# Performance work log

Measured on AMD Instinct MI355X. Metric: run time of the kernel, lower is better.

## Reference

```python
import jax, jax.numpy as jnp
import numpy as np


def setup_inputs() -> dict:
    key = jax.random.key(0)
    ks = jax.random.split(key, 8)
    B, S, V, E, H = 64, 128, 8000, 256, 512
    scale = 0.05
    return {
        "inputs": jax.random.randint(ks[0], (B, S), 0, V, dtype=jnp.int64),
        "embedding": jax.random.normal(ks[1], (V, E), dtype=jnp.float32) * scale,
        "W_ih": jax.random.normal(ks[2], (4 * H, E), dtype=jnp.float32) * scale,
        "W_hh": jax.random.normal(ks[3], (4 * H, H), dtype=jnp.float32) * scale,
        "b_ih": jax.random.normal(ks[4], (4 * H,), dtype=jnp.float32) * scale,
        "b_hh": jax.random.normal(ks[5], (4 * H,), dtype=jnp.float32) * scale,
        "W_cls": jax.random.normal(ks[6], (V, H), dtype=jnp.float32) * scale,
        "b_cls": jax.random.normal(ks[7], (V,), dtype=jnp.float32) * scale,
    }


def reference(inputs, embedding, W_ih, W_hh, b_ih, b_hh, W_cls, b_cls):
    B, S = inputs.shape
    H = W_hh.shape[1]
    x = embedding[inputs]  # (B, S, E)
    # batch the input-to-hidden GEMM across all timesteps
    x_gates = jnp.einsum('bse,ge->bsg', x, W_ih) + b_ih + b_hh  # (B, S, 4H)

    def step(carry, xg):
        h, c = carry
        gates = xg + h @ W_hh.T  # (B, 4H)
        i, f, g, o = jnp.split(gates, 4, axis=-1)  # PyTorch LSTMCell gate order
        i = jax.nn.sigmoid(i)
        f = jax.nn.sigmoid(f)
        g = jnp.tanh(g)
        o = jax.nn.sigmoid(o)
        c = f * c + i * g
        h = o * jnp.tanh(c)
        return (h, c), h

    h0 = jnp.zeros((B, H), dtype=x.dtype)
    c0 = jnp.zeros((B, H), dtype=x.dtype)
    _, hs = jax.lax.scan(step, (h0, c0), jnp.swapaxes(x_gates, 0, 1))  # hs: (S, B, H)
    hidden = jnp.swapaxes(hs, 0, 1)  # (B, S, H)
    logits = jnp.einsum('bsh,vh->bsv', hidden, W_cls) + b_cls  # (B, S, V)
    y = jnp.transpose(logits, (0, 2, 1))  # (B, V, S)
    return jax.nn.log_softmax(y, axis=1)
```

## Files before the change

kernel.cpp:

```cpp
#include <hip/hip_runtime.h>


using u16   = unsigned short;
using u32   = unsigned int;
using u16x8 = __attribute__((ext_vector_type(8))) u16;
using bf16x8 = __attribute__((ext_vector_type(8))) __bf16;
using f32x4 = __attribute__((ext_vector_type(4))) float;

#define NB   64
#define NS   128
#define NV   8000
#define NVP  8192
#define NE   256
#define NH   512
#define NG   2048
#define NBS  8192
#define OUT_BSTRIDE 1024000
#define XG_SSTRIDE  131072

__device__ inline u16 f2bf(float f) {
    unsigned x = __builtin_bit_cast(unsigned, f);
    unsigned r = (x + 0x7FFFu + ((x >> 16) & 1u)) >> 16;
    return (u16)r;
}

__device__ inline bf16x8 ld_frag(const u16* p) {
    u16x8 v = *(const u16x8*)p;
    return __builtin_bit_cast(bf16x8, v);
}

__device__ inline u32 load_llc(const u32* p) {
    u32 v;
    asm volatile("global_load_dword %0, %1, off sc0 sc1\n\t"
                 "s_waitcnt vmcnt(0)"
                 : "=v"(v) : "v"(p) : "memory");
    return v;
}
__device__ inline void load_llc16x2(const void* p0, const void* p1,
                                    f32x4& a, f32x4& b) {
    asm volatile("global_load_dwordx4 %0, %2, off sc0 sc1\n\t"
                 "global_load_dwordx4 %1, %3, off sc0 sc1\n\t"
                 "s_waitcnt vmcnt(0)"
                 : "=&v"(a), "=&v"(b) : "v"(p0), "v"(p1) : "memory");
}
__device__ inline void store_llc(u32* p, u32 v) {
    asm volatile("global_store_dword %0, %1, off sc0 sc1"
                 :: "v"(p), "v"(v) : "memory");
}

__device__ inline void quad_transpose(float v[4], int p) {
    float tb[4];
    #pragma unroll
    for (int q2 = 0; q2 < 4; ++q2) tb[q2] = __shfl_xor(v[q2 ^ 2], 2);
    #pragma unroll
    for (int q2 = 0; q2 < 4; ++q2) v[q2] = (((q2 ^ p) & 2) ? tb[q2] : v[q2]);
    #pragma unroll
    for (int q2 = 0; q2 < 4; ++q2) tb[q2] = __shfl_xor(v[q2 ^ 1], 1);
    #pragma unroll
    for (int q2 = 0; q2 < 4; ++q2) v[q2] = (((q2 ^ p) & 1) ? tb[q2] : v[q2]);
}

__device__ inline float lstm_cell(const float v[4], float& c) {
    float i_ = 1.f / (1.f + __expf(-v[0]));
    float f_ = 1.f / (1.f + __expf(-v[1]));
    float e2 = __expf(2.f * v[2]);
    float g_ = 1.f - 2.f / (e2 + 1.f);
    float o_ = 1.f / (1.f + __expf(-v[3]));
    c = f_ * c + i_ * g_;
    float e2c = __expf(2.f * c);
    return o_ * (1.f - 2.f / (e2c + 1.f));
}

__global__ void cvt_bf16(const float* __restrict__ s, u16* __restrict__ d, int n8) {
    const float4* s4 = (const float4*)s;
    for (int i = blockIdx.x * blockDim.x + threadIdx.x; i < n8;
         i += gridDim.x * blockDim.x) {
        float4 a = s4[2 * i], b = s4[2 * i + 1];
        u16x8 o;
        o[0] = f2bf(a.x); o[1] = f2bf(a.y); o[2] = f2bf(a.z); o[3] = f2bf(a.w);
        o[4] = f2bf(b.x); o[5] = f2bf(b.y); o[6] = f2bf(b.z); o[7] = f2bf(b.w);
        ((u16x8*)d)[i] = o;
    }
}

__global__ __launch_bounds__(256) void k1_xgates(
    const u16* __restrict__ Wih, const u16* __restrict__ emb,
    const int* __restrict__ toks,
    const float* __restrict__ bih, const float* __restrict__ bhh,
    float* __restrict__ xg)
{
    __shared__ u16x8 Al8[512];
    __shared__ u16x8 Bl8[512];
    u16* Al = (u16*)Al8;
    u16* Bl = (u16*)Bl8;

    const int t = threadIdx.x;
    const int lane = t & 63, w = t >> 6;
    const int wm = w >> 1, wn = w & 1;
    const int gtile = blockIdx.y * 128, mtile = blockIdx.x * 128;

    const int r0 = t >> 2, r1 = r0 + 64, q = t & 3;
    const int m0 = mtile + r0, m1 = mtile + r1;
    const int tok0 = toks[(m0 & 63) * NS + (m0 >> 6)];
    const int tok1 = toks[(m1 & 63) * NS + (m1 >> 6)];

    f32x4 acc[4][4];
    for (int i = 0; i < 4; ++i)
        for (int j = 0; j < 4; ++j) acc[i][j] = {0.f, 0.f, 0.f, 0.f};

    const int kc8 = (lane >> 4) * 8;
    for (int kk = 0; kk < 8; ++kk) {
        const int k0 = kk * 32;
        *(u16x8*)&Al[t * 8]         = *(const u16x8*)&Wih[(gtile + r0) * NE + k0 + q * 8];
        *(u16x8*)&Al[(t + 256) * 8] = *(const u16x8*)&Wih[(gtile + r1) * NE + k0 + q * 8];
        *(u16x8*)&Bl[t * 8]         = *(const u16x8*)&emb[tok0 * NE + k0 + q * 8];
        *(u16x8*)&Bl[(t + 256) * 8] = *(const u16x8*)&emb[tok1 * NE + k0 + q * 8];
        __syncthreads();
        bf16x8 af[4], bf[4];
        #pragma unroll
        for (int i = 0; i < 4; ++i) {
            af[i] = ld_frag(&Al[(wm * 64 + i * 16 + (lane & 15)) * 32 + kc8]);
            bf[i] = ld_frag(&Bl[(wn * 64 + i * 16 + (lane & 15)) * 32 + kc8]);
        }
        #pragma unroll
        for (int fi = 0; fi < 4; ++fi)
            #pragma unroll
            for (int fj = 0; fj < 4; ++fj)
                acc[fi][fj] = __builtin_amdgcn_mfma_f32_16x16x32_bf16(
                    af[fi], bf[fj], acc[fi][fj], 0, 0, 0);
        __syncthreads();
    }

    #pragma unroll
    for (int fi = 0; fi < 4; ++fi) {
        const int g0 = gtile + wm * 64 + fi * 16 + ((lane >> 4) << 2);
        const float4 v1 = *(const float4*)&bih[g0];
        const float4 v2 = *(const float4*)&bhh[g0];
        float badd[4] = {v1.x + v2.x, v1.y + v2.y, v1.z + v2.z, v1.w + v2.w};
        #pragma unroll
        for (int fj = 0; fj < 4; ++fj) {
            const int m = mtile + wn * 64 + fj * 16 + (lane & 15);
            const int b = m & 63, s = m >> 6;
            float* dst = &xg[s * XG_SSTRIDE + b];
            #pragma unroll
            for (int r = 0; r < 4; ++r)
                dst[(g0 + r) * 64] = acc[fi][fj][r] + badd[r];
        }
    }
}

#define LSTM_NBLK 32

__global__ __attribute__((amdgpu_flat_work_group_size(512, 512),
                          amdgpu_waves_per_eu(2, 2)))
void k2_lstm(
    const u16* __restrict__ Whh,
    const float* __restrict__ xg,
    u16* __restrict__ hbuf,
    u16* __restrict__ hidden,
    u32* __restrict__ flags)
{
    __shared__ __align__(16) u16 hl[16 * 528];

    const int t = threadIdx.x, lane = t & 63, w = t >> 6;
    const int bg = blockIdx.x >> 3, ug = blockIdx.x & 7;
    const int j = lane & 15;
    const int kc8 = (lane >> 4) * 8;

    const int ubase = ug * 64 + w * 8;
    const int grow0 = (j & 3) * 512 + ubase + (j >> 2);
    const int grow1 = grow0 + 4;

    bf16x8 bw0[16], bw1[16];
    #pragma unroll
    for (int kk = 0; kk < 16; ++kk) {
        bw0[kk] = ld_frag(&Whh[grow0 * NH + kk * 32 + kc8]);
        bw1[kk] = ld_frag(&Whh[grow1 * NH + kk * 32 + kc8]);
    }

    const int srow = t >> 5;
    const int sc   = (t & 31) * 8;
    const int soff = (bg * 16 + srow) * NH + sc;
    u16* hl_w = &hl[srow * 528 + sc];

    const int p  = lane & 3;
    const int q  = (lane >> 2) & 3;
    const int mb = (lane >> 4) * 4;
    const int bat = bg * 16 + mb + p;
    const int un0 = ubase + q;
    const bool sl = ((lane & 4) == 0);

    const int xoff0 = grow0 * 64 + bg * 16 + mb;
    const int xoff1 = grow1 * 64 + bg * 16 + mb;

    float4 xv0 = *(const float4*)&xg[xoff0];
    float4 xv1 = *(const float4*)&xg[xoff1];
    float cA = 0.f, cB = 0.f;

    for (int step = 0; step < NS; ++step) {
        #pragma unroll
        for (int kk = 0; kk < 16; ++kk) {
            f32x4 w0 = __builtin_bit_cast(f32x4, bw0[kk]);
            f32x4 w1 = __builtin_bit_cast(f32x4, bw1[kk]);
            asm volatile("" : "+v"(w0), "+v"(w1));
            bw0[kk] = __builtin_bit_cast(bf16x8, w0);
            bw1[kk] = __builtin_bit_cast(bf16x8, w1);
        }

        float4 xn0 = {0, 0, 0, 0}, xn1 = {0, 0, 0, 0};
        if (step + 1 < NS) {
            const float* xb = &xg[(step + 1) * XG_SSTRIDE];
            xn0 = *(const float4*)&xb[xoff0];
            xn1 = *(const float4*)&xb[xoff1];
        }

        if (step > 0 && lane < 8) {
            const u32* fp = &flags[(bg * 8 + lane) * 32];
            while ((int)load_llc(fp) < step) __builtin_amdgcn_s_sleep(1);
        }
        {
            const u16* hsrc = hbuf + (step & 1) * (NB * NH) + soff;
            f32x4 hA, hB;
            load_llc16x2(hsrc, hsrc + 256, hA, hB);
            *(f32x4*)hl_w = hA;
            *(f32x4*)(hl_w + 256) = hB;
        }
        __syncthreads();

        f32x4 a00 = {0, 0, 0, 0}, a01 = {0, 0, 0, 0};
        f32x4 a10 = {0, 0, 0, 0}, a11 = {0, 0, 0, 0};
        #pragma unroll
        for (int kk = 0; kk < 16; ++kk) {
            bf16x8 av = *(const bf16x8*)&hl[j * 528 + kk * 32 + kc8];
            if (kk & 1) {
                a01 = __builtin_amdgcn_mfma_f32_16x16x32_bf16(av, bw0[kk], a01, 0, 0, 0);
                a11 = __builtin_amdgcn_mfma_f32_16x16x32_bf16(av, bw1[kk], a11, 0, 0, 0);
            } else {
                a00 = __builtin_amdgcn_mfma_f32_16x16x32_bf16(av, bw0[kk], a00, 0, 0, 0);
                a10 = __builtin_amdgcn_mfma_f32_16x16x32_bf16(av, bw1[kk], a10, 0, 0, 0);
            }
        }

        float v0[4], v1[4];
        #pragma unroll
        for (int r = 0; r < 4; ++r) {
            v0[r] = a00[r] + a01[r] + (&xv0.x)[r];
            v1[r] = a10[r] + a11[r] + (&xv1.x)[r];
        }
        quad_transpose(v0, p);
        quad_transpose(v1, p);

        float h0 = lstm_cell(v0, cA);
        float h1 = lstm_cell(v1, cB);
        u32 hb0 = f2bf(h0), hb1 = f2bf(h1);
        u32 o0 = (u32)__shfl_xor((int)hb0, 4);
        u32 o1 = (u32)__shfl_xor((int)hb1, 4);
        u32 p0 = hb0 | (o0 << 16);
        u32 p1 = hb1 | (o1 << 16);
        if (sl) {
            u16* hn = hbuf + ((step & 1) ^ 1) * (NB * NH);
            store_llc((u32*)&hn[bat * NH + un0], p0);
            store_llc((u32*)&hn[bat * NH + un0 + 4], p1);
        }
        xv0 = xn0; xv1 = xn1;
        __syncthreads();

        if (step + 1 < NS && t == 0)
            store_llc(&flags[blockIdx.x * 32], (u32)(step + 1));

        if (sl) {
            *(u32*)&hidden[(bat * NS + step) * NH + un0] = p0;
            *(u32*)&hidden[(bat * NS + step) * NH + un0 + 4] = p1;
        }
    }
}

__global__ __launch_bounds__(256) void k3_cls(
    const u16* __restrict__ Wc, const u16* __restrict__ hid,
    const float* __restrict__ bcls,
    float* __restrict__ out, float* __restrict__ lse)
{
    __shared__ u16x8 Al8[512];
    __shared__ u16x8 Bl8[512];
    __shared__ float red[2][128];
    u16* Al = (u16*)Al8;
    u16* Bl = (u16*)Bl8;

    const int t = threadIdx.x;
    const int lane = t & 63, w = t >> 6;
    const int wm = w >> 1, wn = w & 1;
    const int vtile = blockIdx.y * 128, mtile = blockIdx.x * 128;

    const int r0 = t >> 2, r1 = r0 + 64, q = t & 3;

    f32x4 acc[4][4];
    for (int i = 0; i < 4; ++i)
        for (int j2 = 0; j2 < 4; ++j2) acc[i][j2] = {0.f, 0.f, 0.f, 0.f};

    const int kc8 = (lane >> 4) * 8;
    for (int kk = 0; kk < 16; ++kk) {
        const int k0 = kk * 32;
        *(u16x8*)&Al[t * 8]         = *(const u16x8*)&Wc[(vtile + r0) * NH + k0 + q * 8];
        *(u16x8*)&Al[(t + 256) * 8] = *(const u16x8*)&Wc[(vtile + r1) * NH + k0 + q * 8];
        *(u16x8*)&Bl[t * 8]         = *(const u16x8*)&hid[(mtile + r0) * NH + k0 + q * 8];
        *(u16x8*)&Bl[(t + 256) * 8] = *(const u16x8*)&hid[(mtile + r1) * NH + k0 + q * 8];
        __syncthreads();
        bf16x8 af[4], bf[4];
        #pragma unroll
        for (int i = 0; i < 4; ++i) {
            af[i] = ld_frag(&Al[(wm * 64 + i * 16 + (lane & 15)) * 32 + kc8]);
            bf[i] = ld_frag(&Bl[(wn * 64 + i * 16 + (lane & 15)) * 32 + kc8]);
        }
        #pragma unroll
        for (int fi = 0; fi < 4; ++fi)
            #pragma unroll
            for (int fj = 0; fj < 4; ++fj)
                acc[fi][fj] = __builtin_amdgcn_mfma_f32_16x16x32_bf16(
                    af[fi], bf[fj], acc[fi][fj], 0, 0, 0);
        __syncthreads();
    }

    float lsum[4] = {0.f, 0.f, 0.f, 0.f};
    #pragma unroll
    for (int fi = 0; fi < 4; ++fi) {
        const int v0 = vtile + wm * 64 + fi * 16 + ((lane >> 4) << 2);
        const bool vok = (v0 < NV);
        float4 bc = {0.f, 0.f, 0.f, 0.f};
        if (vok) bc = *(const float4*)&bcls[v0];
        #pragma unroll
        for (int fj = 0; fj < 4; ++fj) {
            const int m = mtile + wn * 64 + fj * 16 + (lane & 15);
            const int b = m >> 7, s = m & 127;
            if (vok) {
                float* dst = &out[b * OUT_BSTRIDE + v0 * NS + s];
                float e = 0.f;
                #pragma unroll
                for (int r = 0; r < 4; ++r) {
                    float lg = acc[fi][fj][r] + (&bc.x)[r];
                    dst[r * NS] = lg;
                    e += __expf(lg);
                }
                lsum[fj] += e;
            }
        }
    }
    #pragma unroll
    for (int fj = 0; fj < 4; ++fj) {
        lsum[fj] += __shfl_xor(lsum[fj], 16);
        lsum[fj] += __shfl_xor(lsum[fj], 32);
    }
    if (lane < 16) {
        #pragma unroll
        for (int fj = 0; fj < 4; ++fj)
            red[wm][wn * 64 + fj * 16 + lane] = lsum[fj];
    }
    __syncthreads();
    if (t < 128) {
        const int m = mtile + t;
        atomicAdd(&lse[m], red[0][t] + red[1][t]);
    }
}

__global__ void k4_log(const float* __restrict__ lse, float* __restrict__ ll) {
    int i = blockIdx.x * 256 + threadIdx.x;
    if (i < NBS) ll[i] = logf(lse[i]);
}

__global__ void k5_norm(float* __restrict__ out, const float* __restrict__ ll) {
    const int total4 = NB * NV * NS / 4;
    float4* o4 = (float4*)out;
    for (int i = blockIdx.x * blockDim.x + threadIdx.x; i < total4;
         i += gridDim.x * blockDim.x) {
        const int i4 = i * 4;
        const int b = i4 / OUT_BSTRIDE;
        const int s = (i4 - b * OUT_BSTRIDE) & 127;
        float4 v = o4[i];
        const float4 l = *(const float4*)&ll[b * NS + s];
        v.x -= l.x; v.y -= l.y; v.z -= l.z; v.w -= l.w;
        o4[i] = v;
    }
}

extern "C" void kernel_launch(void* const* d_in, const int* in_sizes, int n_in,
                              void* d_out, int out_size, void* d_ws, size_t ws_size,
                              hipStream_t stream) {
    const int*   toks   = (const int*)d_in[0];
    const float* emb_f  = (const float*)d_in[1];
    const float* Wih_f  = (const float*)d_in[2];
    const float* Whh_f  = (const float*)d_in[3];
    const float* bih    = (const float*)d_in[4];
    const float* bhh    = (const float*)d_in[5];
    const float* Wcls_f = (const float*)d_in[6];
    const float* bcls   = (const float*)d_in[7];
    float* out = (float*)d_out;
    char*  ws  = (char*)d_ws;

    u32*   flags  = (u32*)(ws + 0);
    float* lse    = (float*)(ws + 8192);
    float* loglse = (float*)(ws + 40960);
    u16*   hbuf   = (u16*)(ws + 73728);
    u16*   embb   = (u16*)(ws + 204800);
    u16*   wihb   = (u16*)(ws + 4300800);
    u16*   whhb   = (u16*)(ws + 5349376);
    u16*   wclsb  = (u16*)(ws + 7446528);
    u16*   hidden = (u16*)(ws + 15835136);

    float* xg = out;

    hipMemsetAsync(ws, 0, 204800, stream);
    hipMemsetAsync((char*)wclsb + NV * NH * 2, 0, (NVP - NV) * NH * 2, stream);

    cvt_bf16<<<1024, 256, 0, stream>>>(emb_f,  embb,  NV * NE / 8);
    cvt_bf16<<<256,  256, 0, stream>>>(Wih_f,  wihb,  NG * NE / 8);
    cvt_bf16<<<512,  256, 0, stream>>>(Whh_f,  whhb,  NG * NH / 8);
    cvt_bf16<<<1024, 256, 0, stream>>>(Wcls_f, wclsb, NV * NH / 8);

    k1_xgates<<<dim3(64, 16), 256, 0, stream>>>(wihb, embb, toks, bih, bhh, xg);
    k2_lstm<<<LSTM_NBLK, 512, 0, stream>>>(whhb, xg, hbuf, hidden, flags);
    k3_cls<<<dim3(64, 64), 256, 0, stream>>>(wclsb, hidden, bcls, out, lse);
    k4_log<<<32, 256, 0, stream>>>(lse, loglse);
    k5_norm<<<2048, 256, 0, stream>>>(out, loglse);
}
```

Before: 712.9 us.

## Replace LSTM flag barrier with step-tagged hidden-state words and LDS double-buffer

The persistent LSTM kernel no longer uses per-block flag words and a spin on them. Each hidden value is now stored as a 32-bit word tagged with its step number, and readers reload any chunk whose tags do not match. This removes one __syncthreads and the separate flag store and poll from each recurrent step, and double-buffers the LDS tile. The hidden exchange doubles in size (32-bit instead of 16-bit per value) and is placed in an unused region of the output buffer. That placement relies on the output buffer being large enough and on k3 later overwriting that region.

After: 876.3 us. 1.23x slower.

```diff
diff --git a/kernel.cpp b/kernel.cpp
--- a/kernel.cpp
+++ b/kernel.cpp
@@ -3,7 +3,9 @@
 
 using u16   = unsigned short;
 using u32   = unsigned int;
+using u16x4 = __attribute__((ext_vector_type(4))) u16;
 using u16x8 = __attribute__((ext_vector_type(8))) u16;
+using u32x4 = __attribute__((ext_vector_type(4))) u32;
 using bf16x8 = __attribute__((ext_vector_type(8))) __bf16;
 using f32x4 = __attribute__((ext_vector_type(4))) float;
 
@@ -29,23 +31,37 @@
     return __builtin_bit_cast(bf16x8, v);
 }
 
-__device__ inline u32 load_llc(const u32* p) {
-    u32 v;
-    asm volatile("global_load_dword %0, %1, off sc0 sc1\n\t"
+__device__ inline void store_llc(u32* p, u32 v) {
+    asm volatile("global_store_dword %0, %1, off sc0 sc1"
+                 :: "v"(p), "v"(v) : "memory");
+}
+__device__ inline u32x4 reload_llc(const u32* p) {
+    u32x4 v;
+    asm volatile("global_load_dwordx4 %0, %1, off sc0 sc1\n\t"
                  "s_waitcnt vmcnt(0)"
                  : "=v"(v) : "v"(p) : "memory");
     return v;
 }
-__device__ inline void load_llc16x2(const void* p0, const void* p1,
-                                    f32x4& a, f32x4& b) {
-    asm volatile("global_load_dwordx4 %0, %2, off sc0 sc1\n\t"
-                 "global_load_dwordx4 %1, %3, off sc0 sc1\n\t"
+__device__ inline void load_llc64(const u32* p, u32x4& a, u32x4& b,
+                                  u32x4& c, u32x4& d) {
+    asm volatile("global_load_dwordx4 %0, %4, off sc0 sc1\n\t"
+                 "global_load_dwordx4 %1, %4, off offset:16 sc0 sc1\n\t"
+                 "global_load_dwordx4 %2, %4, off offset:32 sc0 sc1\n\t"
+                 "global_load_dwordx4 %3, %4, off offset:48 sc0 sc1\n\t"
                  "s_waitcnt vmcnt(0)"
-                 : "=&v"(a), "=&v"(b) : "v"(p0), "v"(p1) : "memory");
-}
-__device__ inline void store_llc(u32* p, u32 v) {
-    asm volatile("global_store_dword %0, %1, off sc0 sc1"
-                 :: "v"(p), "v"(v) : "memory");
+                 : "=&v"(a), "=&v"(b), "=&v"(c), "=&v"(d)
+                 : "v"(p) : "memory");
+}
+
+__device__ inline void commit_chunk(u32x4 v, const u32* src, u16* dst, u32 stp) {
+    for (;;) {
+        u32 bad = ((v[0] >> 16) ^ stp) | ((v[1] >> 16) ^ stp) |
+                  ((v[2] >> 16) ^ stp) | ((v[3] >> 16) ^ stp);
+        if (!bad) break;
+        v = reload_llc(src);
+    }
+    u16x4 h = {(u16)v[0], (u16)v[1], (u16)v[2], (u16)v[3]};
+    *(u16x4*)dst = h;
 }
 
 __device__ inline void quad_transpose(float v[4], int p) {
@@ -156,11 +172,10 @@
 void k2_lstm(
     const u16* __restrict__ Whh,
     const float* __restrict__ xg,
-    u16* __restrict__ hbuf,
-    u16* __restrict__ hidden,
-    u32* __restrict__ flags)
+    u32* __restrict__ thbuf,
+    u16* __restrict__ hidden)
 {
-    __shared__ __align__(16) u16 hl[16 * 528];
+    __shared__ __align__(16) u16 hl[2][16 * 528];
 
     const int t = threadIdx.x, lane = t & 63, w = t >> 6;
     const int bg = blockIdx.x >> 3, ug = blockIdx.x & 7;
@@ -177,11 +192,18 @@
         bw0[kk] = ld_frag(&Whh[grow0 * NH + kk * 32 + kc8]);
         bw1[kk] = ld_frag(&Whh[grow1 * NH + kk * 32 + kc8]);
     }
+    #pragma unroll
+    for (int kk = 0; kk < 16; ++kk) {
+        f32x4 w0 = __builtin_bit_cast(f32x4, bw0[kk]);
+        f32x4 w1 = __builtin_bit_cast(f32x4, bw1[kk]);
+        asm volatile("" : "+v"(w0), "+v"(w1));
+        bw0[kk] = __builtin_bit_cast(bf16x8, w0);
+        bw1[kk] = __builtin_bit_cast(bf16x8, w1);
+    }
 
     const int srow = t >> 5;
-    const int sc   = (t & 31) * 8;
-    const int soff = (bg * 16 + srow) * NH + sc;
-    u16* hl_w = &hl[srow * 528 + sc];
+    const int scb  = (t & 31) * 16;
+    const int soff = (bg * 16 + srow) * NH + scb;
 
     const int p  = lane & 3;
     const int q  = (lane >> 2) & 3;
@@ -198,15 +220,6 @@
     float cA = 0.f, cB = 0.f;
 
     for (int step = 0; step < NS; ++step) {
-        #pragma unroll
-        for (int kk = 0; kk < 16; ++kk) {
-            f32x4 w0 = __builtin_bit_cast(f32x4, bw0[kk]);
-            f32x4 w1 = __builtin_bit_cast(f32x4, bw1[kk]);
-            asm volatile("" : "+v"(w0), "+v"(w1));
-            bw0[kk] = __builtin_bit_cast(bf16x8, w0);
-            bw1[kk] = __builtin_bit_cast(bf16x8, w1);
-        }
-
         float4 xn0 = {0, 0, 0, 0}, xn1 = {0, 0, 0, 0};
         if (step + 1 < NS) {
             const float* xb = &xg[(step + 1) * XG_SSTRIDE];
@@ -214,30 +227,31 @@
             xn1 = *(const float4*)&xb[xoff1];
         }
 
-        if (step > 0 && lane < 8) {
-            const u32* fp = &flags[(bg * 8 + lane) * 32];
-            while ((int)load_llc(fp) < step) __builtin_amdgcn_s_sleep(1);
-        }
-        {
-            const u16* hsrc = hbuf + (step & 1) * (NB * NH) + soff;
-            f32x4 hA, hB;
-            load_llc16x2(hsrc, hsrc + 256, hA, hB);
-            *(f32x4*)hl_w = hA;
-            *(f32x4*)(hl_w + 256) = hB;
-        }
-        __syncthreads();
-
         f32x4 a00 = {0, 0, 0, 0}, a01 = {0, 0, 0, 0};
         f32x4 a10 = {0, 0, 0, 0}, a11 = {0, 0, 0, 0};
-        #pragma unroll
-        for (int kk = 0; kk < 16; ++kk) {
-            bf16x8 av = *(const bf16x8*)&hl[j * 528 + kk * 32 + kc8];
-            if (kk & 1) {
-                a01 = __builtin_amdgcn_mfma_f32_16x16x32_bf16(av, bw0[kk], a01, 0, 0, 0);
-                a11 = __builtin_amdgcn_mfma_f32_16x16x32_bf16(av, bw1[kk], a11, 0, 0, 0);
-            } else {
-                a00 = __builtin_amdgcn_mfma_f32_16x16x32_bf16(av, bw0[kk], a00, 0, 0, 0);
-                a10 = __builtin_amdgcn_mfma_f32_16x16x32_bf16(av, bw1[kk], a10, 0, 0, 0);
+
+        if (step > 0) {
+            const int par = step & 1;
+            const u32* src = thbuf + par * (NB * NH) + soff;
+            u16* dst = &hl[par][srow * 528 + scb];
+            u32x4 c0, c1, c2, c3;
+            load_llc64(src, c0, c1, c2, c3);
+            commit_chunk(c0, src,      dst,      (u32)step);
+            commit_chunk(c1, src + 4,  dst + 4,  (u32)step);
+            commit_chunk(c2, src + 8,  dst + 8,  (u32)step);
+            commit_chunk(c3, src + 12, dst + 12, (u32)step);
+            __syncthreads();
+
+            #pragma unroll
+            for (int kk = 0; kk < 16; ++kk) {
+                bf16x8 av = *(const bf16x8*)&hl[par][j * 528 + kk * 32 + kc8];
+                if (kk & 1) {
+                    a01 = __builtin_amdgcn_mfma_f32_16x16x32_bf16(av, bw0[kk], a01, 0, 0, 0);
+                    a11 = __builtin_amdgcn_mfma_f32_16x16x32_bf16(av, bw1[kk], a11, 0, 0, 0);
+                } else {
+                    a00 = __builtin_amdgcn_mfma_f32_16x16x32_bf16(av, bw0[kk], a00, 0, 0, 0);
+                    a10 = __builtin_amdgcn_mfma_f32_16x16x32_bf16(av, bw1[kk], a10, 0, 0, 0);
+                }
             }
         }
 
@@ -253,25 +267,20 @@
         float h0 = lstm_cell(v0, cA);
         float h1 = lstm_cell(v1, cB);
         u32 hb0 = f2bf(h0), hb1 = f2bf(h1);
+
+        if (step + 1 < NS) {
+            u32 tg = (u32)(step + 1) << 16;
+            u32* hp = thbuf + ((step + 1) & 1) * (NB * NH) + bat * NH;
+            store_llc(&hp[un0],     tg | hb0);
+            store_llc(&hp[un0 + 4], tg | hb1);
+        }
         u32 o0 = (u32)__shfl_xor((int)hb0, 4);
         u32 o1 = (u32)__shfl_xor((int)hb1, 4);
-        u32 p0 = hb0 | (o0 << 16);
-        u32 p1 = hb1 | (o1 << 16);
         if (sl) {
-            u16* hn = hbuf + ((step & 1) ^ 1) * (NB * NH);
-            store_llc((u32*)&hn[bat * NH + un0], p0);
-            store_llc((u32*)&hn[bat * NH + un0 + 4], p1);
+            *(u32*)&hidden[(bat * NS + step) * NH + un0]     = hb0 | (o0 << 16);
+            *(u32*)&hidden[(bat * NS + step) * NH + un0 + 4] = hb1 | (o1 << 16);
         }
         xv0 = xn0; xv1 = xn1;
-        __syncthreads();
-
-        if (step + 1 < NS && t == 0)
-            store_llc(&flags[blockIdx.x * 32], (u32)(step + 1));
-
-        if (sl) {
-            *(u32*)&hidden[(bat * NS + step) * NH + un0] = p0;
-            *(u32*)&hidden[(bat * NS + step) * NH + un0 + 4] = p1;
-        }
     }
 }
 
@@ -395,10 +404,8 @@
     float* out = (float*)d_out;
     char*  ws  = (char*)d_ws;
 
-    u32*   flags  = (u32*)(ws + 0);
     float* lse    = (float*)(ws + 8192);
     float* loglse = (float*)(ws + 40960);
-    u16*   hbuf   = (u16*)(ws + 73728);
     u16*   embb   = (u16*)(ws + 204800);
     u16*   wihb   = (u16*)(ws + 4300800);
     u16*   whhb   = (u16*)(ws + 5349376);
@@ -406,8 +413,10 @@
     u16*   hidden = (u16*)(ws + 15835136);
 
     float* xg = out;
-
-    hipMemsetAsync(ws, 0, 204800, stream);
+    u32* thbuf = (u32*)((char*)out + 80u * 1024u * 1024u);
+
+    hipMemsetAsync(ws, 0, 73728, stream);
+    hipMemsetAsync(thbuf, 0, 2 * NB * NH * 4, stream);
     hipMemsetAsync((char*)wclsb + NV * NH * 2, 0, (NVP - NV) * NH * 2, stream);
 
     cvt_bf16<<<1024, 256, 0, stream>>>(emb_f,  embb,  NV * NE / 8);
@@ -416,7 +425,7 @@
     cvt_bf16<<<1024, 256, 0, stream>>>(Wcls_f, wclsb, NV * NH / 8);
 
     k1_xgates<<<dim3(64, 16), 256, 0, stream>>>(wihb, embb, toks, bih, bhh, xg);
-    k2_lstm<<<LSTM_NBLK, 512, 0, stream>>>(whhb, xg, hbuf, hidden, flags);
+    k2_lstm<<<LSTM_NBLK, 512, 0, stream>>>(whhb, xg, thbuf, hidden);
     k3_cls<<<dim3(64, 64), 256, 0, stream>>>(wclsb, hidden, bcls, out, lse);
     k4_log<<<32, 256, 0, stream>>>(lse, loglse);
     k5_norm<<<2048, 256, 0, stream>>>(out, loglse);
```
